# Kernel tuning notes

Hardware: AMD Instinct MI355X
Metric: run time of the kernel (lower is better)

The kernel has to match this reference:

```python
import jax, jax.numpy as jnp
import numpy as np

B, C, H, W = 4, 64, 64, 64


def setup_inputs() -> dict:
    key = jax.random.key(0)
    k1, k2, k3, k4, k5 = jax.random.split(key, 5)
    return {
        "x": jax.random.normal(k1, (B, C, H, W), dtype=jnp.float32),
        "w_qkv": jax.random.normal(k2, (3 * C, C), dtype=jnp.float32) * (1.0 / np.sqrt(C)),
        "b_qkv": jax.random.normal(k3, (3 * C,), dtype=jnp.float32) * 0.02,
        "w_proj": jax.random.normal(k4, (C, C), dtype=jnp.float32) * (1.0 / np.sqrt(C)),
        "b_proj": jax.random.normal(k5, (C,), dtype=jnp.float32) * 0.02,
    }


def reference(x, w_qkv, b_qkv, w_proj, b_proj):
    b, c, h, w = x.shape
    xf = x.reshape(b, c, h * w)                                  # [B, C, N]
    # 1x1 Conv1d == per-position linear over channels
    qkv = jnp.einsum('oc,bcn->bon', w_qkv, xf) + b_qkv[None, :, None]  # [B, 3C, N]
    q, k, v = jnp.split(qkv, 3, axis=1)                          # each [B, C, N]
    scores = jnp.einsum('bcn,bcm->bnm', q, k) / (c ** 0.5)       # [B, N, N]
    attn = jax.nn.softmax(scores, axis=-1)
    out = jnp.einsum('bcm,bnm->bcn', v, attn)                    # [B, C, N]
    out = jnp.einsum('oc,bcn->bon', w_proj, out) + b_proj[None, :, None]
    return out.reshape(b, c, h, w) + x
```

## Files before the change

kernel.cpp:

```cpp
#include <hip/hip_runtime.h>

typedef __bf16 bf16x8 __attribute__((ext_vector_type(8)));
typedef __bf16 bf16x4 __attribute__((ext_vector_type(4)));
typedef __bf16 bf16x2 __attribute__((ext_vector_type(2)));
typedef float f32x4 __attribute__((ext_vector_type(4)));
typedef float f32x16 __attribute__((ext_vector_type(16)));
typedef short s16x4 __attribute__((ext_vector_type(4)));
typedef unsigned int u32x4 __attribute__((ext_vector_type(4)));

#define NB 4
#define NC 64
#define NN 4096
#define SPLIT 8

#define QSCALE (0.125f * 1.44269504088896340736f)

#if __has_builtin(__builtin_amdgcn_exp2f)
#define EXP2(x) __builtin_amdgcn_exp2f(x)
#else
#define EXP2(x) exp2f(x)
#endif

#define GLL16(src, dst)                                                  \
  __builtin_amdgcn_global_load_lds(                                      \
      (const __attribute__((address_space(1))) void*)(src),              \
      (__attribute__((address_space(3))) void*)(dst), 16, 0, 0)

#define PLSWAP(a, b)                                                     \
  asm volatile("v_permlane32_swap_b32 %0, %1" : "+v"(a), "+v"(b))

__global__ __launch_bounds__(256) void qkv_kernel(
    const float* __restrict__ x, const float* __restrict__ wqkv,
    const float* __restrict__ bqkv,
    __bf16* __restrict__ Qg, __bf16* __restrict__ Kg, __bf16* __restrict__ Vg)
{
  const int tid = threadIdx.x;
  const int wave = tid >> 6;
  const int lane = tid & 63;
  const int quad = lane >> 4;
  const int l16 = lane & 15;
  const int b = blockIdx.y;
  const int tsel = blockIdx.z;
  const int n0 = blockIdx.x * 128 + wave * 32;
  const float wscale = (tsel == 0) ? QSCALE : 1.0f;

  bf16x8 wf[4][2];
#pragma unroll
  for (int ot = 0; ot < 4; ot++) {
#pragma unroll
    for (int ch = 0; ch < 2; ch++) {
      const float* wp =
          wqkv + (size_t)(tsel * 64 + ot * 16 + l16) * 64 + ch * 32 + quad * 8;
      const float4 w0 = *(const float4*)wp;
      const float4 w1 = *(const float4*)(wp + 4);
      bf16x8 f;
      f[0] = (__bf16)(w0.x * wscale); f[1] = (__bf16)(w0.y * wscale);
      f[2] = (__bf16)(w0.z * wscale); f[3] = (__bf16)(w0.w * wscale);
      f[4] = (__bf16)(w1.x * wscale); f[5] = (__bf16)(w1.y * wscale);
      f[6] = (__bf16)(w1.z * wscale); f[7] = (__bf16)(w1.w * wscale);
      wf[ot][ch] = f;
    }
  }
  float bv[4];
#pragma unroll
  for (int ot = 0; ot < 4; ot++)
    bv[ot] = bqkv[tsel * 64 + ot * 16 + l16] * wscale;

#pragma unroll
  for (int nt = 0; nt < 2; nt++) {
    const int nb = n0 + nt * 16 + l16;

    bf16x8 xf[2];
#pragma unroll
    for (int ch = 0; ch < 2; ch++) {
      float v[8];
#pragma unroll
      for (int j = 0; j < 8; j++)
        v[j] = x[(size_t)(b * 64 + ch * 32 + quad * 8 + j) * NN + nb];
      bf16x8 f;
#pragma unroll
      for (int j = 0; j < 8; j++) f[j] = (__bf16)v[j];
      xf[ch] = f;
    }

#pragma unroll
    for (int ot = 0; ot < 4; ot++) {
      f32x4 acc = (f32x4){bv[ot], bv[ot], bv[ot], bv[ot]};
      acc = __builtin_amdgcn_mfma_f32_16x16x32_bf16(xf[0], wf[ot][0], acc, 0, 0, 0);
      acc = __builtin_amdgcn_mfma_f32_16x16x32_bf16(xf[1], wf[ot][1], acc, 0, 0, 0);

      if (tsel < 2) {
        __bf16* dst = (tsel == 0) ? Qg : Kg;
#pragma unroll
        for (int r = 0; r < 4; r++)
          dst[(size_t)(b * NN + n0 + nt * 16 + quad * 4 + r) * 64 + ot * 16 + l16] =
              (__bf16)acc[r];
      } else {
        bf16x4 pv;
#pragma unroll
        for (int r = 0; r < 4; r++) pv[r] = (__bf16)acc[r];
        *(bf16x4*)(Vg + (size_t)(b * 64 + ot * 16 + l16) * NN +
                   n0 + nt * 16 + quad * 4) = pv;
      }
    }
  }
}

__global__ __launch_bounds__(256, 2) void flash_kernel(
    const __bf16* __restrict__ Q, const __bf16* __restrict__ K,
    const __bf16* __restrict__ V, const float* __restrict__ wproj,
    __bf16* __restrict__ Opart, float* __restrict__ lpart)
{
  const int b = blockIdx.y;
  const int s = blockIdx.z;
  const int tid = threadIdx.x;
  const int wave = tid >> 6;
  const int lane = tid & 63;
  const int l32 = lane & 31;
  const int h = lane >> 5;

  __shared__ __bf16 KB[2][64 * 64];
  __shared__ __bf16 VB[2][64 * 64];

  const int q0 = blockIdx.x * 128 + wave * 32;

  bf16x8 qf[4];
  {
    const __bf16* qrow = Q + ((size_t)(b * NN + q0 + l32)) * 64 + h * 8;
    qf[0] = *(const bf16x8*)(qrow);
    qf[1] = *(const bf16x8*)(qrow + 16);
    qf[2] = *(const bf16x8*)(qrow + 32);
    qf[3] = *(const bf16x8*)(qrow + 48);
  }

  int koff[4];
#pragma unroll
  for (int i = 0; i < 4; i++) koff[i] = ((2 * i + h) ^ (lane & 7)) << 3;

  const int c0 = wave * 128 + lane;
  const int c1 = c0 + 64;
  const int r0 = c0 >> 3, r1 = c1 >> 3;
  const int k0 = (c0 & 7) ^ (r0 & 7);
  const int k1 = (c1 & 7) ^ (r1 & 7);
  const int kbeg = s * (NN / SPLIT);
  const __bf16* Ks0 = K + ((size_t)b * NN + kbeg + r0) * 64 + k0 * 8;
  const __bf16* Ks1 = K + ((size_t)b * NN + kbeg + r1) * 64 + k1 * 8;
  const __bf16* Vs0 = V + ((size_t)(b * 64 + r0)) * NN + kbeg + k0 * 8;
  const __bf16* Vs1 = V + ((size_t)(b * 64 + r1)) * NN + kbeg + k1 * 8;
  const int db0 = wave * 1024;
  const int db1 = db0 + 512;

#define STAGE(BUF, T)                                                    \
  {                                                                      \
    GLL16(Ks0 + (size_t)(T) * 4096, &KB[BUF][db0]);                      \
    GLL16(Ks1 + (size_t)(T) * 4096, &KB[BUF][db1]);                      \
    GLL16(Vs0 + (T) * 64, &VB[BUF][db0]);                                \
    GLL16(Vs1 + (T) * 64, &VB[BUF][db1]);                                \
  }

  f32x16 oacc[2] = {};
  float l = 0.f;

  STAGE(0, 0);
  __syncthreads();

#define TILE_COMPUTE(BUF)                                                \
  {                                                                      \
    _Pragma("unroll")                                                    \
    for (int kg = 0; kg < 2; kg++) {                                     \
      f32x16 sa = {};                                                    \
      _Pragma("unroll")                                                  \
      for (int cs = 0; cs < 4; cs++) {                                   \
        const bf16x8 kf =                                                \
            *(const bf16x8*)(&KB[BUF][(kg * 32 + l32) * 64 + koff[cs]]); \
        sa = __builtin_amdgcn_mfma_f32_32x32x16_bf16(kf, qf[cs], sa, 0, 0, 0); \
      }                                                                  \
      _Pragma("unroll")                                                  \
      for (int i = 0; i < 16; i++) sa[i] = EXP2(sa[i]);                  \
      l += ((sa[0] + sa[1]) + (sa[2] + sa[3])) +                         \
           ((sa[4] + sa[5]) + (sa[6] + sa[7])) +                         \
           ((sa[8] + sa[9]) + (sa[10] + sa[11])) +                       \
           ((sa[12] + sa[13]) + (sa[14] + sa[15]));                      \
      unsigned w[8];                                                     \
      _Pragma("unroll")                                                  \
      for (int i = 0; i < 8; i++) {                                      \
        bf16x2 t2;                                                       \
        t2[0] = (__bf16)sa[2 * i]; t2[1] = (__bf16)sa[2 * i + 1];        \
        w[i] = __builtin_bit_cast(unsigned, t2);                         \
      }                                                                  \
      PLSWAP(w[0], w[2]);                                                \
      PLSWAP(w[1], w[3]);                                                \
      PLSWAP(w[4], w[6]);                                                \
      PLSWAP(w[5], w[7]);                                                \
      __builtin_amdgcn_sched_barrier(0);                                 \
      const u32x4 bw0 = (u32x4){w[0], w[1], w[2], w[3]};                 \
      const u32x4 bw1 = (u32x4){w[4], w[5], w[6], w[7]};                 \
      _Pragma("unroll")                                                  \
      for (int cg = 0; cg < 2; cg++) {                                   \
        const bf16x8 va0 = *(const bf16x8*)(                             \
            &VB[BUF][(cg * 32 + l32) * 64 + koff[kg * 2]]);              \
        oacc[cg] = __builtin_amdgcn_mfma_f32_32x32x16_bf16(              \
            va0, __builtin_bit_cast(bf16x8, bw0), oacc[cg], 0, 0, 0);    \
        const bf16x8 va1 = *(const bf16x8*)(                             \
            &VB[BUF][(cg * 32 + l32) * 64 + koff[kg * 2 + 1]]);          \
        oacc[cg] = __builtin_amdgcn_mfma_f32_32x32x16_bf16(              \
            va1, __builtin_bit_cast(bf16x8, bw1), oacc[cg], 0, 0, 0);    \
      }                                                                  \
    }                                                                    \
  }

  const int NT = (NN / SPLIT) / 64;
#pragma unroll 1
  for (int t = 0; t < NT; t += 2) {
    if (t + 1 < NT) STAGE(1, t + 1);
    TILE_COMPUTE(0);
    __syncthreads();
    if (t + 2 < NT) STAGE(0, t + 2);
    TILE_COMPUTE(1);
    if (t + 2 < NT) __syncthreads();
  }

  l += __shfl_xor(l, 32);
  if (h == 0)
    lpart[((size_t)(s * NB + b)) * NN + q0 + l32] = l;

  u32x4 ow[4];
#pragma unroll
  for (int cg = 0; cg < 2; cg++) {
    unsigned w[8];
#pragma unroll
    for (int i = 0; i < 8; i++) {
      bf16x2 t2;
      t2[0] = (__bf16)oacc[cg][2 * i]; t2[1] = (__bf16)oacc[cg][2 * i + 1];
      w[i] = __builtin_bit_cast(unsigned, t2);
    }
    PLSWAP(w[0], w[2]);
    PLSWAP(w[1], w[3]);
    PLSWAP(w[4], w[6]);
    PLSWAP(w[5], w[7]);
    __builtin_amdgcn_sched_barrier(0);
    ow[cg * 2]     = (u32x4){w[0], w[1], w[2], w[3]};
    ow[cg * 2 + 1] = (u32x4){w[4], w[5], w[6], w[7]};
  }

#pragma unroll
  for (int cog = 0; cog < 2; cog++) {
    f32x16 po = {};
#pragma unroll
    for (int cs = 0; cs < 4; cs++) {
      const float* wp = wproj + (size_t)(cog * 32 + l32) * 64 + cs * 16 + h * 8;
      const float4 w0 = *(const float4*)wp;
      const float4 w1 = *(const float4*)(wp + 4);
      bf16x8 wa;
      wa[0] = (__bf16)w0.x; wa[1] = (__bf16)w0.y;
      wa[2] = (__bf16)w0.z; wa[3] = (__bf16)w0.w;
      wa[4] = (__bf16)w1.x; wa[5] = (__bf16)w1.y;
      wa[6] = (__bf16)w1.z; wa[7] = (__bf16)w1.w;
      po = __builtin_amdgcn_mfma_f32_32x32x16_bf16(
          wa, __builtin_bit_cast(bf16x8, ow[cs]), po, 0, 0, 0);
    }
#pragma unroll
    for (int reg = 0; reg < 16; reg++) {
      const int co = cog * 32 + (reg & 3) + 8 * (reg >> 2) + 4 * h;
      Opart[(((size_t)(s * NB + b)) * 64 + co) * NN + q0 + l32] =
          (__bf16)po[reg];
    }
  }
#undef STAGE
#undef TILE_COMPUTE
}

__global__ __launch_bounds__(256) void combine_kernel(
    const __bf16* __restrict__ Opart, const float* __restrict__ lpart,
    const float* __restrict__ bproj, const float* __restrict__ x,
    float* __restrict__ out)
{
  const int b = blockIdx.y;
  const int n0 = blockIdx.x * 32;
  const int tid = threadIdx.x;

  __shared__ float linv[32];
  if (tid < 32) {
    float lt = 0.f;
#pragma unroll
    for (int s = 0; s < SPLIT; s++)
      lt += lpart[((size_t)(s * NB + b)) * NN + n0 + tid];
    linv[tid] = 1.0f / lt;
  }
  __syncthreads();

  const int c = tid >> 2;
  const int n8 = (tid & 3) * 8;

  float o[8];
#pragma unroll
  for (int j = 0; j < 8; j++) o[j] = 0.f;
#pragma unroll
  for (int s = 0; s < SPLIT; s++) {
    const bf16x8 v = *(const bf16x8*)(
        Opart + (((size_t)(s * NB + b)) * 64 + c) * NN + n0 + n8);
#pragma unroll
    for (int j = 0; j < 8; j++) o[j] += (float)v[j];
  }

  const float bb = bproj[c];
  const float4 li0 = *(const float4*)&linv[n8];
  const float4 li1 = *(const float4*)&linv[n8 + 4];
  const size_t base = ((size_t)(b * 64 + c)) * NN + n0 + n8;
  const float4 x0 = *(const float4*)&x[base];
  const float4 x1 = *(const float4*)&x[base + 4];
  float4 r0, r1;
  r0.x = o[0] * li0.x + bb + x0.x;  r0.y = o[1] * li0.y + bb + x0.y;
  r0.z = o[2] * li0.z + bb + x0.z;  r0.w = o[3] * li0.w + bb + x0.w;
  r1.x = o[4] * li1.x + bb + x1.x;  r1.y = o[5] * li1.y + bb + x1.y;
  r1.z = o[6] * li1.z + bb + x1.z;  r1.w = o[7] * li1.w + bb + x1.w;
  *(float4*)&out[base] = r0;
  *(float4*)&out[base + 4] = r1;
}

extern "C" void kernel_launch(void* const* d_in, const int* in_sizes, int n_in,
                              void* d_out, int out_size, void* d_ws, size_t ws_size,
                              hipStream_t stream) {
  const float* x     = (const float*)d_in[0];
  const float* wqkv  = (const float*)d_in[1];
  const float* bqkv  = (const float*)d_in[2];
  const float* wproj = (const float*)d_in[3];
  const float* bproj = (const float*)d_in[4];
  float* out = (float*)d_out;

  char* ws = (char*)d_ws;
  __bf16* Q     = (__bf16*)(ws);
  __bf16* K     = (__bf16*)(ws + (2u << 20));
  __bf16* V     = (__bf16*)(ws + (4u << 20));
  __bf16* Opart = (__bf16*)(ws + (6u << 20));
  float*  lpart = (float*)(ws + (23u << 20));

  qkv_kernel<<<dim3(32, NB, 3), 256, 0, stream>>>(x, wqkv, bqkv, Q, K, V);
  flash_kernel<<<dim3(32, NB, SPLIT), 256, 0, stream>>>(Q, K, V, wproj,
                                                        Opart, lpart);
  combine_kernel<<<dim3(128, NB), 256, 0, stream>>>(Opart, lpart, bproj, x,
                                                    out);
}
```

Baseline: 107.4 us.

## Fuse QKV projections per block, sum softmax denominator with bf16 dot2, drop sched barriers

The QKV kernel now loads each x tile once and loops over Q, K and V weights inside the block, instead of launching separate blocks per projection that each re-read x. In the flash kernel, the row-sum of exponentials is computed with fdot2 on the packed bf16 values, replacing 16 fp32 adds. This also makes the denominator consistent with the bf16-rounded probabilities fed to the PV matmul. Two sched_barrier calls are removed to give the compiler more freedom to schedule. Risks are a small numerical change in l, and a QKV kernel with fewer, more serialized blocks.

After: 106.7 us. No clear change (-0.7%).

```diff
diff --git a/kernel.cpp b/kernel.cpp
--- a/kernel.cpp
+++ b/kernel.cpp
@@ -19,6 +19,12 @@
 #define EXP2(x) __builtin_amdgcn_exp2f(x)
 #else
 #define EXP2(x) exp2f(x)
+#endif
+
+#if __has_builtin(__builtin_amdgcn_fdot2_f32_bf16)
+#define HAVE_FDOT2 1
+#else
+#define HAVE_FDOT2 0
 #endif
 
 #define GLL16(src, dst)                                                  \
@@ -40,48 +46,47 @@
   const int quad = lane >> 4;
   const int l16 = lane & 15;
   const int b = blockIdx.y;
-  const int tsel = blockIdx.z;
-  const int n0 = blockIdx.x * 128 + wave * 32;
-  const float wscale = (tsel == 0) ? QSCALE : 1.0f;
-
-  bf16x8 wf[4][2];
-#pragma unroll
-  for (int ot = 0; ot < 4; ot++) {
-#pragma unroll
-    for (int ch = 0; ch < 2; ch++) {
-      const float* wp =
-          wqkv + (size_t)(tsel * 64 + ot * 16 + l16) * 64 + ch * 32 + quad * 8;
-      const float4 w0 = *(const float4*)wp;
-      const float4 w1 = *(const float4*)(wp + 4);
-      bf16x8 f;
-      f[0] = (__bf16)(w0.x * wscale); f[1] = (__bf16)(w0.y * wscale);
-      f[2] = (__bf16)(w0.z * wscale); f[3] = (__bf16)(w0.w * wscale);
-      f[4] = (__bf16)(w1.x * wscale); f[5] = (__bf16)(w1.y * wscale);
-      f[6] = (__bf16)(w1.z * wscale); f[7] = (__bf16)(w1.w * wscale);
-      wf[ot][ch] = f;
-    }
-  }
-  float bv[4];
-#pragma unroll
-  for (int ot = 0; ot < 4; ot++)
-    bv[ot] = bqkv[tsel * 64 + ot * 16 + l16] * wscale;
-
-#pragma unroll
-  for (int nt = 0; nt < 2; nt++) {
-    const int nb = n0 + nt * 16 + l16;
-
-    bf16x8 xf[2];
-#pragma unroll
-    for (int ch = 0; ch < 2; ch++) {
-      float v[8];
-#pragma unroll
-      for (int j = 0; j < 8; j++)
-        v[j] = x[(size_t)(b * 64 + ch * 32 + quad * 8 + j) * NN + nb];
-      bf16x8 f;
-#pragma unroll
-      for (int j = 0; j < 8; j++) f[j] = (__bf16)v[j];
-      xf[ch] = f;
-    }
+  const int n0 = blockIdx.x * 64 + wave * 16;
+  const int nb = n0 + l16;
+
+  bf16x8 xf[2];
+#pragma unroll
+  for (int ch = 0; ch < 2; ch++) {
+    float v[8];
+#pragma unroll
+    for (int j = 0; j < 8; j++)
+      v[j] = x[(size_t)(b * 64 + ch * 32 + quad * 8 + j) * NN + nb];
+    bf16x8 f;
+#pragma unroll
+    for (int j = 0; j < 8; j++) f[j] = (__bf16)v[j];
+    xf[ch] = f;
+  }
+
+#pragma unroll 1
+  for (int tsel = 0; tsel < 3; tsel++) {
+    const float wscale = (tsel == 0) ? QSCALE : 1.0f;
+
+    bf16x8 wf[4][2];
+#pragma unroll
+    for (int ot = 0; ot < 4; ot++) {
+#pragma unroll
+      for (int ch = 0; ch < 2; ch++) {
+        const float* wp =
+            wqkv + (size_t)(tsel * 64 + ot * 16 + l16) * 64 + ch * 32 + quad * 8;
+        const float4 w0 = *(const float4*)wp;
+        const float4 w1 = *(const float4*)(wp + 4);
+        bf16x8 f;
+        f[0] = (__bf16)(w0.x * wscale); f[1] = (__bf16)(w0.y * wscale);
+        f[2] = (__bf16)(w0.z * wscale); f[3] = (__bf16)(w0.w * wscale);
+        f[4] = (__bf16)(w1.x * wscale); f[5] = (__bf16)(w1.y * wscale);
+        f[6] = (__bf16)(w1.z * wscale); f[7] = (__bf16)(w1.w * wscale);
+        wf[ot][ch] = f;
+      }
+    }
+    float bv[4];
+#pragma unroll
+    for (int ot = 0; ot < 4; ot++)
+      bv[ot] = bqkv[tsel * 64 + ot * 16 + l16] * wscale;
 
 #pragma unroll
     for (int ot = 0; ot < 4; ot++) {
@@ -93,14 +98,14 @@
         __bf16* dst = (tsel == 0) ? Qg : Kg;
 #pragma unroll
         for (int r = 0; r < 4; r++)
-          dst[(size_t)(b * NN + n0 + nt * 16 + quad * 4 + r) * 64 + ot * 16 + l16] =
+          dst[(size_t)(b * NN + n0 + quad * 4 + r) * 64 + ot * 16 + l16] =
               (__bf16)acc[r];
       } else {
         bf16x4 pv;
 #pragma unroll
         for (int r = 0; r < 4; r++) pv[r] = (__bf16)acc[r];
         *(bf16x4*)(Vg + (size_t)(b * 64 + ot * 16 + l16) * NN +
-                   n0 + nt * 16 + quad * 4) = pv;
+                   n0 + quad * 4) = pv;
       }
     }
   }
@@ -133,6 +138,10 @@
     qf[3] = *(const bf16x8*)(qrow + 48);
   }
 
+#if HAVE_FDOT2
+  const bf16x2 ones2 = {(__bf16)1.0f, (__bf16)1.0f};
+#endif
+
   int koff[4];
 #pragma unroll
   for (int i = 0; i < 4; i++) koff[i] = ((2 * i + h) ^ (lane & 7)) << 3;
@@ -177,10 +186,6 @@
       }                                                                  \
       _Pragma("unroll")                                                  \
       for (int i = 0; i < 16; i++) sa[i] = EXP2(sa[i]);                  \
-      l += ((sa[0] + sa[1]) + (sa[2] + sa[3])) +                         \
-           ((sa[4] + sa[5]) + (sa[6] + sa[7])) +                         \
-           ((sa[8] + sa[9]) + (sa[10] + sa[11])) +                       \
-           ((sa[12] + sa[13]) + (sa[14] + sa[15]));                      \
       unsigned w[8];                                                     \
       _Pragma("unroll")                                                  \
       for (int i = 0; i < 8; i++) {                                      \
@@ -188,11 +193,11 @@
         t2[0] = (__bf16)sa[2 * i]; t2[1] = (__bf16)sa[2 * i + 1];        \
         w[i] = __builtin_bit_cast(unsigned, t2);                         \
       }                                                                  \
+      LSUM_BLOCK(sa, w)                                                  \
       PLSWAP(w[0], w[2]);                                                \
       PLSWAP(w[1], w[3]);                                                \
       PLSWAP(w[4], w[6]);                                                \
       PLSWAP(w[5], w[7]);                                                \
-      __builtin_amdgcn_sched_barrier(0);                                 \
       const u32x4 bw0 = (u32x4){w[0], w[1], w[2], w[3]};                 \
       const u32x4 bw1 = (u32x4){w[4], w[5], w[6], w[7]};                 \
       _Pragma("unroll")                                                  \
@@ -209,6 +214,20 @@
     }                                                                    \
   }
 
+#if HAVE_FDOT2
+#define LSUM_BLOCK(sa, w)                                                \
+      _Pragma("unroll")                                                  \
+      for (int i = 0; i < 8; i++)                                        \
+        l = __builtin_amdgcn_fdot2_f32_bf16(                             \
+            __builtin_bit_cast(bf16x2, w[i]), ones2, l, false);
+#else
+#define LSUM_BLOCK(sa, w)                                                \
+      l += ((sa[0] + sa[1]) + (sa[2] + sa[3])) +                         \
+           ((sa[4] + sa[5]) + (sa[6] + sa[7])) +                         \
+           ((sa[8] + sa[9]) + (sa[10] + sa[11])) +                       \
+           ((sa[12] + sa[13]) + (sa[14] + sa[15]));
+#endif
+
   const int NT = (NN / SPLIT) / 64;
 #pragma unroll 1
   for (int t = 0; t < NT; t += 2) {
@@ -238,7 +257,6 @@
     PLSWAP(w[1], w[3]);
     PLSWAP(w[4], w[6]);
     PLSWAP(w[5], w[7]);
-    __builtin_amdgcn_sched_barrier(0);
     ow[cg * 2]     = (u32x4){w[0], w[1], w[2], w[3]};
     ow[cg * 2 + 1] = (u32x4){w[4], w[5], w[6], w[7]};
   }
@@ -268,6 +286,7 @@
   }
 #undef STAGE
 #undef TILE_COMPUTE
+#undef LSUM_BLOCK
 }
 
 __global__ __launch_bounds__(256) void combine_kernel(
@@ -335,7 +354,7 @@
   __bf16* Opart = (__bf16*)(ws + (6u << 20));
   float*  lpart = (float*)(ws + (23u << 20));
 
-  qkv_kernel<<<dim3(32, NB, 3), 256, 0, stream>>>(x, wqkv, bqkv, Q, K, V);
+  qkv_kernel<<<dim3(64, NB), 256, 0, stream>>>(x, wqkv, bqkv, Q, K, V);
   flash_kernel<<<dim3(32, NB, SPLIT), 256, 0, stream>>>(Q, K, V, wproj,
                                                         Opart, lpart);
   combine_kernel<<<dim3(128, NB), 256, 0, stream>>>(Opart, lpart, bproj, x,
```
